# Kernel optimization log

Hardware: AMD Instinct MI355X
Metric: run time of the kernel (lower is better)

Reference implementation:

```python
import jax, jax.numpy as jnp
import numpy as np

B, T, C, H = 8, 2048, 1024, 64

def setup_inputs() -> dict:
    key = jax.random.key(0)
    k1, k2, k3, k4 = jax.random.split(key, 4)
    x = jax.random.normal(k1, (B, T, C), dtype=jnp.float32)
    sw = 1.0 / np.sqrt(C)  # Linear-like init scale
    Wq = jax.random.normal(k2, (C, H), dtype=jnp.float32) * sw
    Wk = jax.random.normal(k3, (C, H), dtype=jnp.float32) * sw
    Wv = jax.random.normal(k4, (C, H), dtype=jnp.float32) * sw
    return {"x": x, "Wq": Wq, "Wk": Wk, "Wv": Wv}

def reference(x, Wq, Wk, Wv):
    # Single-head causal self-attention (eval mode: dropout is identity).
    # Quantized GEMMs (QLinear / qmatmul) are represented by exact fp32 math.
    Bx, Tx, Cx = x.shape
    q = jnp.einsum('btc,ch->bth', x, Wq)          # [B,T,H]
    k = jnp.einsum('btc,ch->bth', x, Wk)          # [B,T,H]
    v = jnp.einsum('btc,ch->bth', x, Wv)          # [B,T,H]
    scale = k.shape[-1] ** -0.5
    wei = jnp.einsum('bth,bsh->bts', q, k) * scale  # [B,T,T]
    causal = jnp.tril(jnp.ones((Tx, Tx), dtype=bool))
    wei = jnp.where(causal, wei, -jnp.inf)
    wei = jax.nn.softmax(wei, axis=-1)
    out = jnp.einsum('bts,bsh->bth', wei, v)      # [B,T,H]
    return out
```

## Files before the change

kernel.cpp:

```cpp
#include <hip/hip_runtime.h>
#include <math.h>

#define Bz 8
#define Tz 2048
#define Cz 1024
#define Hz 64
#define BT (Bz*Tz)

typedef __attribute__((ext_vector_type(8))) short bf16x8;
typedef __attribute__((ext_vector_type(4))) float f32x4;
typedef __attribute__((ext_vector_type(4))) unsigned short us4;

#define PSTRIDE 4160

__device__ __forceinline__ unsigned short f2bf(float f) {
    union { float f; unsigned u; } v; v.f = f;
    unsigned r = v.u + 0x7fffu + ((v.u >> 16) & 1u);
    return (unsigned short)(r >> 16);
}

__device__ __forceinline__ bf16x8 pack8(const float* s) {
    bf16x8 r;
#pragma unroll
    for (int j = 0; j < 8; j++) r[j] = (short)f2bf(s[j]);
    return r;
}

__device__ __forceinline__ bf16x8 pack8f4(float4 a, float4 b) {
    bf16x8 r;
    r[0] = (short)f2bf(a.x); r[1] = (short)f2bf(a.y);
    r[2] = (short)f2bf(a.z); r[3] = (short)f2bf(a.w);
    r[4] = (short)f2bf(b.x); r[5] = (short)f2bf(b.y);
    r[6] = (short)f2bf(b.z); r[7] = (short)f2bf(b.w);
    return r;
}

__device__ __forceinline__ void gload16(const void* g, void* l) {
    __builtin_amdgcn_global_load_lds(
        (const __attribute__((address_space(1))) void*)g,
        (__attribute__((address_space(3))) void*)l, 16, 0, 0);
}

__global__ __launch_bounds__(256)
void wprep_kernel(const float* __restrict__ Wq, const float* __restrict__ Wk,
                  const float* __restrict__ Wv, unsigned short* __restrict__ Wti)
{
    __shared__ float T[64][65];
    const int mat = blockIdx.x >> 4;
    const int kt  = blockIdx.x & 15;
    const int k0  = kt * 64;
    const float* W = (mat == 0) ? Wq : (mat == 1) ? Wk : Wv;
    const int t  = threadIdx.x;
    const int rr = t >> 2;
    const int c4 = (t & 3) * 16;
#pragma unroll
    for (int j = 0; j < 4; j++) {
        float4 w4 = *(const float4*)&W[(size_t)(k0 + rr) * Hz + c4 + j * 4];
        T[c4 + j*4 + 0][rr] = w4.x;
        T[c4 + j*4 + 1][rr] = w4.y;
        T[c4 + j*4 + 2][rr] = w4.z;
        T[c4 + j*4 + 3][rr] = w4.w;
    }
    __syncthreads();
    const int nn  = t >> 2;
    const int sl0 = (t & 3) * 2;
    const int n   = mat * 64 + nn;
    float tmp[16];
#pragma unroll
    for (int j = 0; j < 16; j++) tmp[j] = T[nn][sl0 * 8 + j];
    unsigned short* base = &Wti[(size_t)kt * 12288 + n * 64];
    *(bf16x8*)&base[((sl0    ) ^ (n & 7)) * 8] = pack8(tmp);
    *(bf16x8*)&base[((sl0 + 1) ^ (n & 7)) * 8] = pack8(tmp + 8);
}

__global__ __launch_bounds__(256, 2)
void qkv_mfma_kernel(const float* __restrict__ x, const unsigned short* __restrict__ Wti,
                     unsigned short* __restrict__ qg, unsigned short* __restrict__ kg,
                     unsigned short* __restrict__ vT)
{
    __shared__ __align__(16) float          xsF[2][32 * 64];
    __shared__ __align__(16) unsigned short ws [2][192 * 64];

    const int t    = threadIdx.x;
    const int M0   = blockIdx.x * 32;
    const int ln   = t & 15;
    const int g    = (t & 63) >> 4;
    const int g4   = g * 4;
    const int w    = t >> 6;
    const int wr   = w & 1;
    const int wc   = w >> 1;
    const int lane = t & 63;
    const float SCq = 0.18033688011112042f;

    f32x4 acc[6];
#pragma unroll
    for (int i = 0; i < 6; i++) acc[i] = (f32x4){0.f, 0.f, 0.f, 0.f};

    auto issue = [&](int buf, int kt) {
        const int k0 = kt * 64;
#pragma unroll
        for (int j = 0; j < 2; j++) {
            const int r  = w * 8 + j * 4 + (lane >> 4);
            const int sl = (lane & 15) ^ (r & 7);
            gload16(&x[(size_t)(M0 + r) * Cz + k0 + sl * 4],
                    &xsF[buf][(w * 8 + j * 4) * 64]);
        }
#pragma unroll
        for (int j = 0; j < 6; j++) {
            const int jj = w * 6 + j;
            gload16(&Wti[(size_t)kt * 12288 + jj * 512 + lane * 8],
                    &ws[buf][jj * 512]);
        }
    };

    issue(0, 0);
    __syncthreads();
    int cur = 0;

    for (int kt = 0; kt < 16; kt++) {
        if (kt < 15) issue(cur ^ 1, kt + 1);

        bf16x8 af[2];
        const int row = wr * 16 + ln;
#pragma unroll
        for (int kc = 0; kc < 2; kc++) {
            const int s0 = kc * 8 + g * 2;
            float4 fa = *(const float4*)&xsF[cur][row * 64 + ((s0    ) ^ (row & 7)) * 4];
            float4 fb = *(const float4*)&xsF[cur][row * 64 + ((s0 + 1) ^ (row & 7)) * 4];
            af[kc] = pack8f4(fa, fb);
        }
        __builtin_amdgcn_s_setprio(1);
#pragma unroll
        for (int ct = 0; ct < 6; ct++) {
            const int nn = wc * 96 + ct * 16 + ln;
#pragma unroll
            for (int kc = 0; kc < 2; kc++) {
                bf16x8 bf = *(const bf16x8*)&ws[cur][nn * 64 + ((kc*4 + g) ^ (nn & 7)) * 8];
                acc[ct] = __builtin_amdgcn_mfma_f32_16x16x32_bf16(af[kc], bf, acc[ct], 0, 0, 0);
            }
        }
        __builtin_amdgcn_s_setprio(0);
        __syncthreads();
        cur ^= 1;
    }

#pragma unroll
    for (int ct = 0; ct < 6; ct++) {
        const int col0 = wc * 96 + ct * 16;
        const int mat  = col0 >> 6;
        const int cl   = (col0 & 63) + ln;
        const int m0   = M0 + wr * 16 + g4;
        if (mat == 0) {
#pragma unroll
            for (int i = 0; i < 4; i++)
                qg[(size_t)(m0 + i) * Hz + cl] = f2bf(acc[ct][i] * SCq);
        } else if (mat == 1) {
#pragma unroll
            for (int i = 0; i < 4; i++)
                kg[(size_t)(m0 + i) * Hz + cl] = f2bf(acc[ct][i]);
        } else {
            const int b = m0 >> 11, tt = m0 & 2047;
            us4 pk;
#pragma unroll
            for (int i = 0; i < 4; i++) pk[i] = f2bf(acc[ct][i]);
            *(us4*)&vT[((size_t)b * Hz + cl) * Tz + tt] = pk;
        }
    }
}

template<int S>
__global__ __launch_bounds__(256, 4)
void attn_mfma_kernel(const unsigned short* __restrict__ qg,
                      const unsigned short* __restrict__ kg,
                      const unsigned short* __restrict__ vT,
                      float* __restrict__ pbase)
{
    __shared__ __align__(16) unsigned short Ks [2][64 * 64];
    __shared__ __align__(16) unsigned short Vts[2][64 * 64];
    __shared__ __align__(16) unsigned short Ps [4 * 16 * 64];

    const int bid = blockIdx.x;
    const int b   = bid & 7;
    const int r0  = bid >> 3;
    const int c   = r0 % S;
    const int qt  = 31 - (r0 / S);
    if (c > qt) return;
    const int q0  = qt * 64;

    const int t  = threadIdx.x;
    const int ln = t & 15;
    const int g  = (t & 63) >> 4;
    const int g4 = g * 4;
    const int w  = t >> 6;
    const int l6 = t & 63;

    const unsigned short* qb = qg + (size_t)b * Tz * Hz;
    const unsigned short* kb = kg + (size_t)b * Tz * Hz;
    const unsigned short* vb = vT + (size_t)b * Hz * Tz;

    const int rl  = l6 >> 3;
    const int swz = ((l6 & 7) ^ rl) * 8;
    auto issue_tile = [&](int buf, int s0) {
#pragma unroll
        for (int qq = 0; qq < 2; qq++) {
            const int row = w*16 + qq*8 + rl;
            gload16(&kb[(size_t)(s0 + row) * Hz + swz],
                    &Ks[buf][(w*16 + qq*8) * 64]);
            gload16(&vb[(size_t)row * Tz + s0 + swz],
                    &Vts[buf][(w*16 + qq*8) * 64]);
        }
    };

    issue_tile(0, c * 64);

    bf16x8 qf[2];
    {
        const int qrow = q0 + w*16 + ln;
        qf[0] = *(const bf16x8*)&qb[(size_t)qrow * Hz + g*8];
        qf[1] = *(const bf16x8*)&qb[(size_t)qrow * Hz + 32 + g*8];
    }

    f32x4 accO[4];
#pragma unroll
    for (int i = 0; i < 4; i++) accO[i] = (f32x4){0.f, 0.f, 0.f, 0.f};
    float lrow = 0.f;
    unsigned short* Pw = &Ps[w * 1024];
    const int pwbase = ln*64 + (g & 1) * 4;
    const int pslotx = (g >> 1);

    __syncthreads();
    int cur = 0;

    for (int s = c; s <= qt; s += S) {
        if (s + S <= qt) issue_tile(cur ^ 1, (s + S) * 64);

        const unsigned short* Kc = &Ks[cur][0];
        const unsigned short* Vc = &Vts[cur][0];

        f32x4 accS[4];
        __builtin_amdgcn_s_setprio(1);
#pragma unroll
        for (int t4 = 0; t4 < 4; t4++) {
            accS[t4] = (f32x4){0.f, 0.f, 0.f, 0.f};
#pragma unroll
            for (int kc = 0; kc < 2; kc++) {
                const int n = t4*16 + ln;
                bf16x8 kf = *(const bf16x8*)&Kc[n*64 + ((kc*4 + g) ^ (n & 7)) * 8];
                accS[t4] = __builtin_amdgcn_mfma_f32_16x16x32_bf16(kf, qf[kc], accS[t4], 0, 0, 0);
            }
        }
        __builtin_amdgcn_s_setprio(0);

        const bool diag = (s == qt);
        float lp0 = 0.f, lp1 = 0.f;
#pragma unroll
        for (int t4 = 0; t4 < 4; t4++) {
            us4 pk;
#pragma unroll
            for (int i = 0; i < 4; i++) {
                float sv = accS[t4][i];
                if (diag && (t4*16 + g4 + i > w*16 + ln)) sv = -1e30f;
                const float p = exp2f(sv);
                if (t4 & 1) lp1 += p; else lp0 += p;
                pk[i] = f2bf(p);
            }
            *(us4*)&Pw[pwbase + ((t4*2 + pslotx) ^ (ln & 7)) * 8] = pk;
        }
        lrow += lp0 + lp1;

        __builtin_amdgcn_s_setprio(1);
#pragma unroll
        for (int kc = 0; kc < 2; kc++) {
            bf16x8 pa = *(const bf16x8*)&Pw[ln*64 + ((kc*4 + g) ^ (ln & 7)) * 8];
#pragma unroll
            for (int ht = 0; ht < 4; ht++) {
                const int vr2 = ht*16 + ln;
                bf16x8 vf = *(const bf16x8*)&Vc[vr2*64 + ((kc*4 + g) ^ (vr2 & 7)) * 8];
                accO[ht] = __builtin_amdgcn_mfma_f32_16x16x32_bf16(pa, vf, accO[ht], 0, 0, 0);
            }
        }
        __builtin_amdgcn_s_setprio(0);

        __syncthreads();
        cur ^= 1;
    }

    lrow += __shfl_xor(lrow, 16);
    lrow += __shfl_xor(lrow, 32);

    float* Op = pbase + (size_t)((b * 32 + qt) * S + c) * PSTRIDE;
#pragma unroll
    for (int ht = 0; ht < 4; ht++)
#pragma unroll
        for (int i = 0; i < 4; i++)
            Op[(size_t)(w*16 + g4 + i) * 64 + ht*16 + ln] = accO[ht][i];
    if (g == 0)
        Op[4096 + w*16 + ln] = lrow;
}

template<int S>
__global__ __launch_bounds__(256)
void combine_kernel(const float* __restrict__ pbase, float* __restrict__ out)
{
    const int bid = blockIdx.x;
    const int b   = bid & 7;
    const int qt  = 31 - (bid >> 3);
    const int t   = threadIdx.x;
    const int r   = t >> 2;
    const int cg  = t & 3;

    const int nch = (qt + 1 < S) ? (qt + 1) : S;
    const float* P0 = pbase + (size_t)(b * 32 + qt) * S * PSTRIDE;

    float denom = 0.f;
    float4 o[4];
#pragma unroll
    for (int j = 0; j < 4; j++) o[j] = make_float4(0.f, 0.f, 0.f, 0.f);
    for (int cc = 0; cc < nch; cc++) {
        const float* Pc = P0 + (size_t)cc * PSTRIDE;
        denom += Pc[4096 + r];
#pragma unroll
        for (int j = 0; j < 4; j++) {
            float4 v4 = *(const float4*)&Pc[(size_t)r * 64 + cg * 16 + j * 4];
            o[j].x += v4.x; o[j].y += v4.y; o[j].z += v4.z; o[j].w += v4.w;
        }
    }
    const float inv = 1.f / denom;
    float* ob = out + ((size_t)b * Tz + qt * 64 + r) * Hz + cg * 16;
#pragma unroll
    for (int j = 0; j < 4; j++)
        *(float4*)&ob[j * 4] = make_float4(o[j].x * inv, o[j].y * inv,
                                           o[j].z * inv, o[j].w * inv);
}

extern "C" void kernel_launch(void* const* d_in, const int* in_sizes, int n_in,
                              void* d_out, int out_size, void* d_ws, size_t ws_size,
                              hipStream_t stream) {
    const float* x  = (const float*)d_in[0];
    const float* Wq = (const float*)d_in[1];
    const float* Wk = (const float*)d_in[2];
    const float* Wv = (const float*)d_in[3];

    unsigned short* Wti = (unsigned short*)d_ws;
    unsigned short* qg  = Wti + 196608;
    unsigned short* kg  = qg + (size_t)BT * Hz;
    unsigned short* vT  = kg + (size_t)BT * Hz;
    const size_t baseShorts = 196608 + 3 * (size_t)BT * Hz;
    float* pbase = (float*)((char*)d_ws + baseShorts * 2);
    float* out = (float*)d_out;

    wprep_kernel<<<48, 256, 0, stream>>>(Wq, Wk, Wv, Wti);
    qkv_mfma_kernel<<<BT / 32, 256, 0, stream>>>(x, Wti, qg, kg, vT);

    const size_t base = baseShorts * 2;
    const size_t per  = (size_t)8 * 32 * PSTRIDE * 4;
    if (ws_size >= base + 4 * per) {
        attn_mfma_kernel<4><<<8 * 32 * 4, 256, 0, stream>>>(qg, kg, vT, pbase);
        combine_kernel<4><<<256, 256, 0, stream>>>(pbase, out);
    } else {
        attn_mfma_kernel<1><<<8 * 32 * 1, 256, 0, stream>>>(qg, kg, vT, pbase);
        combine_kernel<1><<<256, 256, 0, stream>>>(pbase, out);
    }
}
```

Measured before the change: 50.45 us.

## Fuse split-K combine into attention kernel via last-block atomic counter

```diff
diff --git a/kernel.cpp b/kernel.cpp
--- a/kernel.cpp
+++ b/kernel.cpp
@@ -1,4 +1,5 @@
 #include <hip/hip_runtime.h>
+#include <hip/hip_bf16.h>
 #include <math.h>
 
 #define Bz 8
@@ -14,9 +15,10 @@
 #define PSTRIDE 4160
 
 __device__ __forceinline__ unsigned short f2bf(float f) {
-    union { float f; unsigned u; } v; v.f = f;
-    unsigned r = v.u + 0x7fffu + ((v.u >> 16) & 1u);
-    return (unsigned short)(r >> 16);
+    __hip_bfloat16 h = __float2bfloat16(f);
+    unsigned short u;
+    __builtin_memcpy(&u, &h, 2);
+    return u;
 }
 
 __device__ __forceinline__ bf16x8 pack8(const float* s) {
@@ -173,7 +175,8 @@
 void attn_mfma_kernel(const unsigned short* __restrict__ qg,
                       const unsigned short* __restrict__ kg,
                       const unsigned short* __restrict__ vT,
-                      float* __restrict__ pbase)
+                      float* __restrict__ pbase, int* __restrict__ cnt,
+                      float* __restrict__ out)
 {
     __shared__ __align__(16) unsigned short Ks [2][64 * 64];
     __shared__ __align__(16) unsigned short Vts[2][64 * 64];
@@ -296,41 +299,40 @@
             Op[(size_t)(w*16 + g4 + i) * 64 + ht*16 + ln] = accO[ht][i];
     if (g == 0)
         Op[4096 + w*16 + ln] = lrow;
-}
-
-template<int S>
-__global__ __launch_bounds__(256)
-void combine_kernel(const float* __restrict__ pbase, float* __restrict__ out)
-{
-    const int bid = blockIdx.x;
-    const int b   = bid & 7;
-    const int qt  = 31 - (bid >> 3);
-    const int t   = threadIdx.x;
-    const int r   = t >> 2;
-    const int cg  = t & 3;
 
     const int nch = (qt + 1 < S) ? (qt + 1) : S;
-    const float* P0 = pbase + (size_t)(b * 32 + qt) * S * PSTRIDE;
-
-    float denom = 0.f;
-    float4 o[4];
-#pragma unroll
-    for (int j = 0; j < 4; j++) o[j] = make_float4(0.f, 0.f, 0.f, 0.f);
-    for (int cc = 0; cc < nch; cc++) {
-        const float* Pc = P0 + (size_t)cc * PSTRIDE;
-        denom += Pc[4096 + r];
-#pragma unroll
-        for (int j = 0; j < 4; j++) {
-            float4 v4 = *(const float4*)&Pc[(size_t)r * 64 + cg * 16 + j * 4];
-            o[j].x += v4.x; o[j].y += v4.y; o[j].z += v4.z; o[j].w += v4.w;
-        }
-    }
-    const float inv = 1.f / denom;
-    float* ob = out + ((size_t)b * Tz + qt * 64 + r) * Hz + cg * 16;
-#pragma unroll
-    for (int j = 0; j < 4; j++)
-        *(float4*)&ob[j * 4] = make_float4(o[j].x * inv, o[j].y * inv,
-                                           o[j].z * inv, o[j].w * inv);
+    __shared__ int lastflag;
+    __threadfence();
+    __syncthreads();
+    if (t == 0) {
+        const int old = atomicAdd(&cnt[b * 32 + qt], 1);
+        lastflag = (old == nch - 1) ? 1 : 0;
+    }
+    __syncthreads();
+    if (lastflag) {
+        const float* P0 = pbase + (size_t)(b * 32 + qt) * S * PSTRIDE;
+        const int r  = t >> 2;
+        const int cg = t & 3;
+        float denom = 0.f;
+        float4 o[4];
+#pragma unroll
+        for (int j = 0; j < 4; j++) o[j] = make_float4(0.f, 0.f, 0.f, 0.f);
+        for (int cc = 0; cc < nch; cc++) {
+            const float* Pc = P0 + (size_t)cc * PSTRIDE;
+            denom += Pc[4096 + r];
+#pragma unroll
+            for (int j = 0; j < 4; j++) {
+                float4 v4 = *(const float4*)&Pc[(size_t)r * 64 + cg * 16 + j * 4];
+                o[j].x += v4.x; o[j].y += v4.y; o[j].z += v4.z; o[j].w += v4.w;
+            }
+        }
+        const float inv = 1.f / denom;
+        float* ob = out + ((size_t)b * Tz + q0 + r) * Hz + cg * 16;
+#pragma unroll
+        for (int j = 0; j < 4; j++)
+            *(float4*)&ob[j * 4] = make_float4(o[j].x * inv, o[j].y * inv,
+                                               o[j].z * inv, o[j].w * inv);
+    }
 }
 
 extern "C" void kernel_launch(void* const* d_in, const int* in_sizes, int n_in,
@@ -346,19 +348,19 @@
     unsigned short* kg  = qg + (size_t)BT * Hz;
     unsigned short* vT  = kg + (size_t)BT * Hz;
     const size_t baseShorts = 196608 + 3 * (size_t)BT * Hz;
-    float* pbase = (float*)((char*)d_ws + baseShorts * 2);
+    int*   cnt   = (int*)((char*)d_ws + baseShorts * 2);
+    float* pbase = (float*)((char*)cnt + 1024);
     float* out = (float*)d_out;
 
+    hipMemsetAsync(cnt, 0, 256 * sizeof(int), stream);
     wprep_kernel<<<48, 256, 0, stream>>>(Wq, Wk, Wv, Wti);
     qkv_mfma_kernel<<<BT / 32, 256, 0, stream>>>(x, Wti, qg, kg, vT);
 
-    const size_t base = baseShorts * 2;
+    const size_t base = baseShorts * 2 + 1024;
     const size_t per  = (size_t)8 * 32 * PSTRIDE * 4;
     if (ws_size >= base + 4 * per) {
-        attn_mfma_kernel<4><<<8 * 32 * 4, 256, 0, stream>>>(qg, kg, vT, pbase);
-        combine_kernel<4><<<256, 256, 0, stream>>>(pbase, out);
+        attn_mfma_kernel<4><<<8 * 32 * 4, 256, 0, stream>>>(qg, kg, vT, pbase, cnt, out);
     } else {
-        attn_mfma_kernel<1><<<8 * 32 * 1, 256, 0, stream>>>(qg, kg, vT, pbase);
-        combine_kernel<1><<<256, 256, 0, stream>>>(pbase, out);
-    }
-}
+        attn_mfma_kernel<1><<<8 * 32 * 1, 256, 0, stream>>>(qg, kg, vT, pbase, cnt, out);
+    }
+}
```

Result: slower. 167.9 us (+232.8%).

## Load x directly into registers and use hardware bf16 pack conversion

Applied to the files above, without the earlier changes.

```diff
diff --git a/kernel.cpp b/kernel.cpp
--- a/kernel.cpp
+++ b/kernel.cpp
@@ -26,13 +26,19 @@
     return r;
 }
 
-__device__ __forceinline__ bf16x8 pack8f4(float4 a, float4 b) {
-    bf16x8 r;
-    r[0] = (short)f2bf(a.x); r[1] = (short)f2bf(a.y);
-    r[2] = (short)f2bf(a.z); r[3] = (short)f2bf(a.w);
-    r[4] = (short)f2bf(b.x); r[5] = (short)f2bf(b.y);
-    r[6] = (short)f2bf(b.z); r[7] = (short)f2bf(b.w);
+__device__ __forceinline__ unsigned cvt_pk_bf16(float lo, float hi) {
+    unsigned r;
+    asm volatile("v_cvt_pk_bf16_f32 %0, %1, %2" : "=v"(r) : "v"(lo), "v"(hi));
     return r;
+}
+
+__device__ __forceinline__ bf16x8 cvt8(float4 a, float4 b) {
+    union { unsigned u[4]; bf16x8 v; } r;
+    r.u[0] = cvt_pk_bf16(a.x, a.y);
+    r.u[1] = cvt_pk_bf16(a.z, a.w);
+    r.u[2] = cvt_pk_bf16(b.x, b.y);
+    r.u[3] = cvt_pk_bf16(b.z, b.w);
+    return r.v;
 }
 
 __device__ __forceinline__ void gload16(const void* g, void* l) {
@@ -73,13 +79,12 @@
     *(bf16x8*)&base[((sl0 + 1) ^ (n & 7)) * 8] = pack8(tmp + 8);
 }
 
-__global__ __launch_bounds__(256, 2)
+__global__ __launch_bounds__(256, 3)
 void qkv_mfma_kernel(const float* __restrict__ x, const unsigned short* __restrict__ Wti,
                      unsigned short* __restrict__ qg, unsigned short* __restrict__ kg,
                      unsigned short* __restrict__ vT)
 {
-    __shared__ __align__(16) float          xsF[2][32 * 64];
-    __shared__ __align__(16) unsigned short ws [2][192 * 64];
+    __shared__ __align__(16) unsigned short ws[2][192 * 64];
 
     const int t    = threadIdx.x;
     const int M0   = blockIdx.x * 32;
@@ -96,15 +101,9 @@
 #pragma unroll
     for (int i = 0; i < 6; i++) acc[i] = (f32x4){0.f, 0.f, 0.f, 0.f};
 
-    auto issue = [&](int buf, int kt) {
-        const int k0 = kt * 64;
-#pragma unroll
-        for (int j = 0; j < 2; j++) {
-            const int r  = w * 8 + j * 4 + (lane >> 4);
-            const int sl = (lane & 15) ^ (r & 7);
-            gload16(&x[(size_t)(M0 + r) * Cz + k0 + sl * 4],
-                    &xsF[buf][(w * 8 + j * 4) * 64]);
-        }
+    const float* xrow = &x[(size_t)(M0 + wr * 16 + ln) * Cz + g * 8];
+
+    auto issueW = [&](int buf, int kt) {
 #pragma unroll
         for (int j = 0; j < 6; j++) {
             const int jj = w * 6 + j;
@@ -113,22 +112,27 @@
         }
     };
 
-    issue(0, 0);
+    float4 xf[4], xfn[4];
+    auto loadX = [&](int kt, float4* d) {
+        const float* p = xrow + kt * 64;
+        d[0] = *(const float4*)(p);
+        d[1] = *(const float4*)(p + 4);
+        d[2] = *(const float4*)(p + 32);
+        d[3] = *(const float4*)(p + 36);
+    };
+
+    issueW(0, 0);
+    loadX(0, xf);
     __syncthreads();
     int cur = 0;
 
     for (int kt = 0; kt < 16; kt++) {
-        if (kt < 15) issue(cur ^ 1, kt + 1);
+        if (kt < 15) { issueW(cur ^ 1, kt + 1); loadX(kt + 1, xfn); }
 
         bf16x8 af[2];
-        const int row = wr * 16 + ln;
-#pragma unroll
-        for (int kc = 0; kc < 2; kc++) {
-            const int s0 = kc * 8 + g * 2;
-            float4 fa = *(const float4*)&xsF[cur][row * 64 + ((s0    ) ^ (row & 7)) * 4];
-            float4 fb = *(const float4*)&xsF[cur][row * 64 + ((s0 + 1) ^ (row & 7)) * 4];
-            af[kc] = pack8f4(fa, fb);
-        }
+        af[0] = cvt8(xf[0], xf[1]);
+        af[1] = cvt8(xf[2], xf[3]);
+
         __builtin_amdgcn_s_setprio(1);
 #pragma unroll
         for (int ct = 0; ct < 6; ct++) {
@@ -141,6 +145,8 @@
         }
         __builtin_amdgcn_s_setprio(0);
         __syncthreads();
+#pragma unroll
+        for (int i = 0; i < 4; i++) xf[i] = xfn[i];
         cur ^= 1;
     }
 
@@ -252,21 +258,22 @@
         __builtin_amdgcn_s_setprio(0);
 
         const bool diag = (s == qt);
-        float lp0 = 0.f, lp1 = 0.f;
 #pragma unroll
         for (int t4 = 0; t4 < 4; t4++) {
-            us4 pk;
+            float pv[4];
 #pragma unroll
             for (int i = 0; i < 4; i++) {
                 float sv = accS[t4][i];
                 if (diag && (t4*16 + g4 + i > w*16 + ln)) sv = -1e30f;
                 const float p = exp2f(sv);
-                if (t4 & 1) lp1 += p; else lp0 += p;
-                pk[i] = f2bf(p);
+                lrow += p;
+                pv[i] = p;
             }
-            *(us4*)&Pw[pwbase + ((t4*2 + pslotx) ^ (ln & 7)) * 8] = pk;
-        }
-        lrow += lp0 + lp1;
+            uint2 pk2;
+            pk2.x = cvt_pk_bf16(pv[0], pv[1]);
+            pk2.y = cvt_pk_bf16(pv[2], pv[3]);
+            *(uint2*)&Pw[pwbase + ((t4*2 + pslotx) ^ (ln & 7)) * 8] = pk2;
+        }
 
         __builtin_amdgcn_s_setprio(1);
 #pragma unroll
```

New measurement: 53.11 us. +5.3%, slower.

## Use hardware bf16 pack conversion and 64-row QKV tiles with 512 threads

Applied to the files above, without the earlier changes.

```diff
diff --git a/kernel.cpp b/kernel.cpp
--- a/kernel.cpp
+++ b/kernel.cpp
@@ -26,13 +26,19 @@
     return r;
 }
 
-__device__ __forceinline__ bf16x8 pack8f4(float4 a, float4 b) {
-    bf16x8 r;
-    r[0] = (short)f2bf(a.x); r[1] = (short)f2bf(a.y);
-    r[2] = (short)f2bf(a.z); r[3] = (short)f2bf(a.w);
-    r[4] = (short)f2bf(b.x); r[5] = (short)f2bf(b.y);
-    r[6] = (short)f2bf(b.z); r[7] = (short)f2bf(b.w);
+__device__ __forceinline__ unsigned cvt_pk_bf16(float lo, float hi) {
+    unsigned r;
+    asm volatile("v_cvt_pk_bf16_f32 %0, %1, %2" : "=v"(r) : "v"(lo), "v"(hi));
     return r;
+}
+
+__device__ __forceinline__ bf16x8 cvt8(float4 a, float4 b) {
+    union { unsigned u[4]; bf16x8 v; } r;
+    r.u[0] = cvt_pk_bf16(a.x, a.y);
+    r.u[1] = cvt_pk_bf16(a.z, a.w);
+    r.u[2] = cvt_pk_bf16(b.x, b.y);
+    r.u[3] = cvt_pk_bf16(b.z, b.w);
+    return r.v;
 }
 
 __device__ __forceinline__ void gload16(const void* g, void* l) {
@@ -73,22 +79,22 @@
     *(bf16x8*)&base[((sl0 + 1) ^ (n & 7)) * 8] = pack8(tmp + 8);
 }
 
-__global__ __launch_bounds__(256, 2)
+__global__ __launch_bounds__(512, 4)
 void qkv_mfma_kernel(const float* __restrict__ x, const unsigned short* __restrict__ Wti,
                      unsigned short* __restrict__ qg, unsigned short* __restrict__ kg,
                      unsigned short* __restrict__ vT)
 {
-    __shared__ __align__(16) float          xsF[2][32 * 64];
+    __shared__ __align__(16) float          xsF[2][64 * 64];
     __shared__ __align__(16) unsigned short ws [2][192 * 64];
 
     const int t    = threadIdx.x;
-    const int M0   = blockIdx.x * 32;
+    const int M0   = blockIdx.x * 64;
     const int ln   = t & 15;
     const int g    = (t & 63) >> 4;
     const int g4   = g * 4;
     const int w    = t >> 6;
-    const int wr   = w & 1;
-    const int wc   = w >> 1;
+    const int rg   = w & 3;
+    const int wc   = w >> 2;
     const int lane = t & 63;
     const float SCq = 0.18033688011112042f;
 
@@ -106,8 +112,8 @@
                     &xsF[buf][(w * 8 + j * 4) * 64]);
         }
 #pragma unroll
-        for (int j = 0; j < 6; j++) {
-            const int jj = w * 6 + j;
+        for (int j = 0; j < 3; j++) {
+            const int jj = w * 3 + j;
             gload16(&Wti[(size_t)kt * 12288 + jj * 512 + lane * 8],
                     &ws[buf][jj * 512]);
         }
@@ -121,13 +127,13 @@
         if (kt < 15) issue(cur ^ 1, kt + 1);
 
         bf16x8 af[2];
-        const int row = wr * 16 + ln;
+        const int row = rg * 16 + ln;
 #pragma unroll
         for (int kc = 0; kc < 2; kc++) {
             const int s0 = kc * 8 + g * 2;
             float4 fa = *(const float4*)&xsF[cur][row * 64 + ((s0    ) ^ (row & 7)) * 4];
             float4 fb = *(const float4*)&xsF[cur][row * 64 + ((s0 + 1) ^ (row & 7)) * 4];
-            af[kc] = pack8f4(fa, fb);
+            af[kc] = cvt8(fa, fb);
         }
         __builtin_amdgcn_s_setprio(1);
 #pragma unroll
@@ -149,7 +155,7 @@
         const int col0 = wc * 96 + ct * 16;
         const int mat  = col0 >> 6;
         const int cl   = (col0 & 63) + ln;
-        const int m0   = M0 + wr * 16 + g4;
+        const int m0   = M0 + rg * 16 + g4;
         if (mat == 0) {
 #pragma unroll
             for (int i = 0; i < 4; i++)
@@ -252,21 +258,22 @@
         __builtin_amdgcn_s_setprio(0);
 
         const bool diag = (s == qt);
-        float lp0 = 0.f, lp1 = 0.f;
 #pragma unroll
         for (int t4 = 0; t4 < 4; t4++) {
-            us4 pk;
+            float pv[4];
 #pragma unroll
             for (int i = 0; i < 4; i++) {
                 float sv = accS[t4][i];
                 if (diag && (t4*16 + g4 + i > w*16 + ln)) sv = -1e30f;
                 const float p = exp2f(sv);
-                if (t4 & 1) lp1 += p; else lp0 += p;
-                pk[i] = f2bf(p);
+                lrow += p;
+                pv[i] = p;
             }
-            *(us4*)&Pw[pwbase + ((t4*2 + pslotx) ^ (ln & 7)) * 8] = pk;
-        }
-        lrow += lp0 + lp1;
+            uint2 pk2;
+            pk2.x = cvt_pk_bf16(pv[0], pv[1]);
+            pk2.y = cvt_pk_bf16(pv[2], pv[3]);
+            *(uint2*)&Pw[pwbase + ((t4*2 + pslotx) ^ (ln & 7)) * 8] = pk2;
+        }
 
         __builtin_amdgcn_s_setprio(1);
 #pragma unroll
@@ -350,7 +357,7 @@
     float* out = (float*)d_out;
 
     wprep_kernel<<<48, 256, 0, stream>>>(Wq, Wk, Wv, Wti);
-    qkv_mfma_kernel<<<BT / 32, 256, 0, stream>>>(x, Wti, qg, kg, vT);
+    qkv_mfma_kernel<<<BT / 64, 512, 0, stream>>>(x, Wti, qg, kg, vT);
 
     const size_t base = baseShorts * 2;
     const size_t per  = (size_t)8 * 32 * PSTRIDE * 4;
```

New measurement: 52.32 us. 1.04x slower.
